# Kernel tuning notes

Measured on AMD Instinct MI355X. Metric: run time of the kernel, lower is better.

The kernel has to match this reference:

```python
import jax, jax.numpy as jnp
import numpy as np

N, E = 100000, 1600000
IN_CH, HID, HEADS, OUT_CH = 128, 32, 2, 40
NEG_SLOPE = 0.2
BN_EPS = 1e-5


def _param(key, shape, scale=0.1):
    return scale * jax.random.normal(key, shape, dtype=jnp.float32)


def setup_inputs() -> dict:
    key = jax.random.key(0)
    ks = jax.random.split(key, 24)
    x = jax.random.normal(ks[0], (N, IN_CH), dtype=jnp.float32)
    edge_index = jax.random.randint(ks[1], (2, E), 0, N, dtype=jnp.int32)
    d0 = HEADS * HID  # 64
    inp = {
        'x': x, 'edge_index': edge_index,
        # conv0: in 128 -> 32 per head, concat -> 64
        'W0': _param(ks[2], (IN_CH, HEADS * HID)),
        'as0': _param(ks[3], (HEADS, HID)), 'ad0': _param(ks[4], (HEADS, HID)),
        'b0': jnp.zeros((d0,), jnp.float32),
        'g0': jnp.ones((d0,), jnp.float32), 'bt0': jnp.zeros((d0,), jnp.float32),
        # conv1: 64 -> 32 per head, concat -> 64
        'W1': _param(ks[5], (d0, HEADS * HID)),
        'as1': _param(ks[6], (HEADS, HID)), 'ad1': _param(ks[7], (HEADS, HID)),
        'b1': jnp.zeros((d0,), jnp.float32),
        'g1': jnp.ones((d0,), jnp.float32), 'bt1': jnp.zeros((d0,), jnp.float32),
        # conv2: 64 -> 40 per head, mean over heads -> 40
        'W2': _param(ks[8], (d0, HEADS * OUT_CH)),
        'as2': _param(ks[9], (HEADS, OUT_CH)), 'ad2': _param(ks[10], (HEADS, OUT_CH)),
        'b2': jnp.zeros((OUT_CH,), jnp.float32),
    }
    return inp


def gat_conv(x, src, dst, W, a_src, a_dst, bias, out_ch, concat):
    n = x.shape[0]
    h = (x @ W).reshape(n, HEADS, out_ch)            # [N,H,C]
    alpha_src = jnp.sum(h * a_src, axis=-1)          # [N,H]
    alpha_dst = jnp.sum(h * a_dst, axis=-1)          # [N,H]
    e = jax.nn.leaky_relu(alpha_src[src] + alpha_dst[dst], NEG_SLOPE)  # [E,H]
    # softmax over incoming edges per destination node (self loops guarantee >=1 edge)
    m = jax.ops.segment_max(e, dst, num_segments=n)
    e = jnp.exp(e - m[dst])
    s = jax.ops.segment_sum(e, dst, num_segments=n)
    alpha = e / s[dst]                                # [E,H]
    msg = h[src] * alpha[:, :, None]                  # [E,H,C]
    out = jax.ops.segment_sum(msg, dst, num_segments=n)  # [N,H,C]
    out = out.reshape(n, HEADS * out_ch) if concat else out.mean(axis=1)
    return out + bias


def batch_norm(x, gamma, beta):
    mu = jnp.mean(x, axis=0)
    var = jnp.mean(jnp.square(x - mu), axis=0)
    return gamma * (x - mu) * jax.lax.rsqrt(var + BN_EPS) + beta


def reference(x, edge_index, W0, as0, ad0, b0, g0, bt0,
              W1, as1, ad1, b1, g1, bt1, W2, as2, ad2, b2):
    n = x.shape[0]
    loops = jnp.arange(n, dtype=edge_index.dtype)
    src = jnp.concatenate([edge_index[0], loops])
    dst = jnp.concatenate([edge_index[1], loops])
    h = gat_conv(x, src, dst, W0, as0, ad0, b0, HID, True)
    h = jax.nn.elu(batch_norm(h, g0, bt0))
    h = gat_conv(h, src, dst, W1, as1, ad1, b1, HID, True)
    h = jax.nn.elu(batch_norm(h, g1, bt1))
    return gat_conv(h, src, dst, W2, as2, ad2, b2, OUT_CH, False)
```

## Files before the change

kernel.cpp:

```cpp
#include <hip/hip_runtime.h>
#include <hip/hip_bf16.h>
#include <math.h>


#define NNODES 100000
#define NEDGES 1600000
#define ENTOT  (NEDGES + NNODES)
#define NEG_SLOPE 0.2f
#define BN_EPS 1e-5f

#define NRANGE 8
#define RSIZE  (NNODES/NRANGE)
#define BCAP   262144
#define PBLK   2048
#define NB2    32

typedef unsigned short u16;
typedef unsigned int u32;
typedef unsigned long long u64;
typedef __attribute__((ext_vector_type(8))) short short8;
typedef __attribute__((ext_vector_type(4))) float f32x4;

__device__ __forceinline__ float b2f(u16 u){ union{u32 i; float f;} v; v.i=((u32)u)<<16; return v.f; }
__device__ __forceinline__ u16 f2b(float x){ __hip_bfloat16 b=__float2bfloat16(x); return *(u16*)&b; }
__device__ __forceinline__ float ldf(const void* p, int i, int f){
  return f ? ((const float*)p)[i] : b2f(((const u16*)p)[i]);
}

__global__ void k_detect(const u16* __restrict__ x, int* __restrict__ flag){
  __shared__ int bad;
  if(threadIdx.x==0) bad=0;
  __syncthreads();
  int cnt=0;
  for(int i=threadIdx.x;i<4096;i+=256){
    u16 v = x[2*i];
    int ex = (v>>7)&0xff;
    if(ex==0xff || (ex==0 && (v&0x7fff)!=0)) cnt++;
  }
  atomicAdd(&bad,cnt);
  __syncthreads();
  if(threadIdx.x==0) flag[0] = (bad>4)?1:0;
}

__global__ __launch_bounds__(256) void k_part2(
    const int* __restrict__ ei, int* __restrict__ gptr, u32* __restrict__ bkt){
  __shared__ int lcnt[NRANGE], gbase[NRANGE];
  int t=threadIdx.x;
  if(t<NRANGE) lcnt[t]=0;
  __syncthreads();
  const int CH=(ENTOT+PBLK-1)/PBLK;
  int beg=blockIdx.x*CH, end=beg+CH; if(end>ENTOT) end=ENTOT;
  int nd[4], ns[4], nr[4], ne=0;
  for(int i=beg+t; i<end; i+=256){
    int d=(i<NEDGES)? ei[NEDGES+i] : (i-NEDGES);
    int s=(i<NEDGES)? ei[i] : d;
    nd[ne]=d; ns[ne]=s; ne++;
  }
  #pragma unroll 4
  for(int k=0;k<ne;k++) nr[k]=atomicAdd(&lcnt[nd[k]/RSIZE],1);
  __syncthreads();
  if(t<NRANGE) gbase[t]=atomicAdd(&gptr[t],lcnt[t]);
  __syncthreads();
  #pragma unroll 4
  for(int k=0;k<ne;k++){
    int r=nd[k]/RSIZE;
    u32 e = ((u32)(nd[k]-r*RSIZE)<<17) | (u32)ns[k];
    __builtin_nontemporal_store(e, &bkt[(size_t)r*BCAP + gbase[r] + nr[k]]);
  }
}

__global__ __launch_bounds__(256) void k_hist4(
    const u32* __restrict__ bkt, const int* __restrict__ gptr, int* __restrict__ lhist){
  __shared__ int lh[RSIZE];
  int t=threadIdx.x;
  for(int i=t;i<RSIZE;i+=256) lh[i]=0;
  __syncthreads();
  int r = blockIdx.x & (NRANGE-1);
  int c = blockIdx.x >> 3;
  int n = gptr[r];
  int per=(n+NB2-1)/NB2;
  int beg=c*per, end=beg+per; if(end>n) end=n;
  const u32* bp = bkt + (size_t)r*BCAP;
  for(int i=beg+t;i<end;i+=256) atomicAdd(&lh[bp[i]>>17],1);
  __syncthreads();
  int* out = lhist + (size_t)(r*NB2+c)*RSIZE;
  for(int i=t;i<RSIZE;i+=256) out[i]=lh[i];
}

__global__ __launch_bounds__(256) void k_sumscan(int* __restrict__ lhist, int* __restrict__ cnt){
  int n = blockIdx.x*256 + threadIdx.x;
  if(n>=NNODES) return;
  int r = n/RSIZE, i = n - r*RSIZE;
  int* base = lhist + (size_t)r*NB2*RSIZE + i;
  int run=0;
  #pragma unroll 8
  for(int c=0;c<NB2;c++){
    int v = base[(size_t)c*RSIZE];
    base[(size_t)c*RSIZE] = run;
    run += v;
  }
  cnt[n]=run;
}

#define SCAN_M (NNODES+1)
#define SCAN_NB ((SCAN_M + 2047)/2048)

__global__ void k_scan_a(const int* __restrict__ cnt, int* __restrict__ bsum){
  __shared__ int red[256];
  int b=blockIdx.x, t=threadIdx.x;
  int base = b*2048 + t*8;
  int s=0;
  #pragma unroll
  for(int j=0;j<8;j++){ int idx=base+j; s += (idx<NNODES)? cnt[idx]:0; }
  red[t]=s; __syncthreads();
  for(int o=128;o>0;o>>=1){ if(t<o) red[t]+=red[t+o]; __syncthreads(); }
  if(t==0) bsum[b]=red[0];
}

__global__ void k_scan_b(int* bsum){
  if(threadIdx.x==0){
    int run=0;
    for(int i=0;i<SCAN_NB;i++){ int v=bsum[i]; bsum[i]=run; run+=v; }
  }
}

__global__ void k_scan_c(const int* __restrict__ cnt, const int* __restrict__ bsum,
                         int* __restrict__ row_ptr){
  __shared__ int lds[256];
  int b=blockIdx.x, t=threadIdx.x;
  int base=b*2048+t*8;
  int v[8]; int s=0;
  #pragma unroll
  for(int j=0;j<8;j++){ int idx=base+j; int x=(idx<NNODES)?cnt[idx]:0; v[j]=s; s+=x; }
  lds[t]=s; __syncthreads();
  for(int o=1;o<256;o<<=1){
    int other=0; if(t>=o) other=lds[t-o];
    __syncthreads();
    lds[t]+=other;
    __syncthreads();
  }
  int texcl = lds[t] - s;
  int off0 = bsum[b] + texcl;
  #pragma unroll
  for(int j=0;j<8;j++){ int idx=base+j; if(idx<SCAN_M) row_ptr[idx]=off0+v[j]; }
}

__global__ __launch_bounds__(256) void k_scatter4(
    const u32* __restrict__ bkt, const int* __restrict__ gptr,
    const int* __restrict__ row_ptr, const int* __restrict__ lhist,
    int* __restrict__ col){
  __shared__ int lofs[RSIZE];
  int t=threadIdx.x;
  int r = blockIdx.x & (NRANGE-1);
  int c = blockIdx.x >> 3;
  int lo = r*RSIZE;
  const int* cb = lhist + (size_t)(r*NB2+c)*RSIZE;
  for(int i=t;i<RSIZE;i+=256) lofs[i] = row_ptr[lo+i] + cb[i];
  __syncthreads();
  int n = gptr[r];
  int per=(n+NB2-1)/NB2;
  int beg=c*per, end=beg+per; if(end>n) end=n;
  const u32* bp = bkt + (size_t)r*BCAP;
  for(int i=beg+t;i<end;i+=256){
    u32 e=bp[i];
    int pos=atomicAdd(&lofs[e>>17],1);
    col[pos]=(int)(e & 0x1FFFF);
  }
}

template<int K, int OUTC, int HID, bool XEXT, bool BN>
__global__ __launch_bounds__(256) void k_gemm_mfma(
    const void* __restrict__ xin, const void* __restrict__ W,
    const void* __restrict__ avs, const void* __restrict__ avd,
    const float2* __restrict__ bnab,
    u16* __restrict__ hout, float* __restrict__ asrc, float* __restrict__ adst,
    const int* __restrict__ flagp)
{
  const int f = flagp[0];
  constexpr int KP = K+8;
  constexpr int RS = OUTC+8;
  constexpr int NT = OUTC/16;
  constexpr int KQ = K/32;
  __shared__ __align__(16) u16 WT[OUTC*KP];
  __shared__ __align__(16) u16 HROW[4*16*RS];
  __shared__ float AVb[2*OUTC];
  __shared__ float2 BB[K];
  int t=threadIdx.x;
  const u16* Wu=(const u16*)W; const float* Wf=(const float*)W;
  for(int i8=t*8; i8<K*OUTC; i8+=256*8){
    int k=i8/OUTC, c0=i8-k*OUTC;
    u16 w8[8];
    if(f){
      const float* wp=Wf+i8;
      float4 a=*(const float4*)wp, b=*(const float4*)(wp+4);
      w8[0]=f2b(a.x);w8[1]=f2b(a.y);w8[2]=f2b(a.z);w8[3]=f2b(a.w);
      w8[4]=f2b(b.x);w8[5]=f2b(b.y);w8[6]=f2b(b.z);w8[7]=f2b(b.w);
    } else {
      uint4 q=*(const uint4*)(Wu+i8);
      w8[0]=q.x&0xffff;w8[1]=q.x>>16;w8[2]=q.y&0xffff;w8[3]=q.y>>16;
      w8[4]=q.z&0xffff;w8[5]=q.z>>16;w8[6]=q.w&0xffff;w8[7]=q.w>>16;
    }
    #pragma unroll
    for(int u=0;u<8;u++) WT[(c0+u)*KP + k] = w8[u];
  }
  for(int idx=t; idx<2*OUTC; idx+=256)
    AVb[idx] = (idx<OUTC)? ldf(avs,idx,f) : ldf(avd,idx-OUTC,f);
  if(BN) for(int idx=t; idx<K; idx+=256) BB[idx]=bnab[idx];
  __syncthreads();

  int wv=t>>6, lane=t&63;
  int m=lane&15, quad=lane>>4;
  int grow0 = blockIdx.x*64 + wv*16;
  int growA = grow0 + m;
  bool avalid = growA < NNODES;
  int growC = avalid ? growA : 0;

  f32x4 acc[NT] = {};
  #pragma unroll
  for(int kq=0;kq<KQ;kq++){
    int k0 = kq*32 + quad*8;
    union{ u32 u[4]; short8 s8; } A;
    if(XEXT && f==1){
      const float* xr=(const float*)xin + (size_t)growC*K + k0;
      float4 p=*(const float4*)xr, q=*(const float4*)(xr+4);
      A.u[0]=f2b(p.x)|((u32)f2b(p.y)<<16);
      A.u[1]=f2b(p.z)|((u32)f2b(p.w)<<16);
      A.u[2]=f2b(q.x)|((u32)f2b(q.y)<<16);
      A.u[3]=f2b(q.z)|((u32)f2b(q.w)<<16);
    } else {
      uint4 q=*(const uint4*)((const u16*)xin + (size_t)growC*K + k0);
      A.u[0]=q.x; A.u[1]=q.y; A.u[2]=q.z; A.u[3]=q.w;
    }
    if(BN){
      #pragma unroll
      for(int j=0;j<4;j++){
        float lo=b2f(A.u[j]&0xffff), hi=b2f(A.u[j]>>16);
        float2 c1=BB[k0+2*j], c2=BB[k0+2*j+1];
        lo=c1.x*lo+c1.y; lo = lo>0.f? lo : __expf(lo)-1.f;
        hi=c2.x*hi+c2.y; hi = hi>0.f? hi : __expf(hi)-1.f;
        A.u[j]=f2b(lo)|((u32)f2b(hi)<<16);
      }
    }
    #pragma unroll
    for(int nt=0;nt<NT;nt++){
      union{ uint4 q; short8 s8; } Bf;
      Bf.q = *(const uint4*)&WT[(nt*16+m)*KP + k0];
      acc[nt] = __builtin_amdgcn_mfma_f32_16x16x32_bf16(A.s8, Bf.s8, acc[nt], 0,0,0);
    }
  }
  u16* hr = &HROW[wv*16*RS];
  #pragma unroll
  for(int nt=0;nt<NT;nt++){
    #pragma unroll
    for(int reg=0;reg<4;reg++)
      hr[(quad*4+reg)*RS + nt*16+m] = f2b(acc[nt][reg]);
  }
  __syncthreads();
  {
    int row=lane&15, task=quad, head=task&1, sd=task>>1;
    float p=0.f;
    const u16* hrow=&hr[row*RS + head*HID];
    const float* av=&AVb[sd*OUTC + head*HID];
    #pragma unroll 8
    for(int c=0;c<HID;c++) p += b2f(hrow[c])*av[c];
    int grow=grow0+row;
    if(grow<NNODES){ (sd? adst:asrc)[grow*2+head]=p; }
  }
  {
    constexpr int CH8 = OUTC/8;
    for(int idx=lane; idx<16*CH8; idx+=64){
      int rr=idx/CH8, c8=idx-rr*CH8;
      int grow=grow0+rr;
      if(grow<NNODES)
        *(uint4*)(hout + (size_t)grow*OUTC + c8*8) = *(const uint4*)&hr[rr*RS + c8*8];
    }
  }
}

template<int OUTC, bool FINAL>
__global__ __launch_bounds__(256) void k_aggf(
  const int* __restrict__ row_ptr, const int* __restrict__ col,
  const u16* __restrict__ hin, const float2* __restrict__ asrc2,
  const float2* __restrict__ adst2, const void* __restrict__ bias,
  u16* __restrict__ houtb, void* __restrict__ outv, const int* __restrict__ flagp)
{
  const int f = flagp[0];
  __shared__ float vbuf[4][80];
  int wave = threadIdx.x>>6, lane=threadIdx.x&63;
  int rr = blockIdx.x & 7, jb = blockIdx.x >> 3;
  int d = rr*RSIZE + jb*4 + wave;
  int base=row_ptr[d], deg=row_ptr[d+1]-base;
  int slot=lane>>3, cg=lane&7;
  constexpr int HSPLIT = FINAL ? 5 : 4;
  float2 adv = adst2[d];
  float acc[8]={0,0,0,0,0,0,0,0}, accx[2]={0.f,0.f};
  float s0=0.f, s1=0.f;
  for(int j=0;j<deg;j+=8){
    int jj=j+slot;
    bool valid = jj<deg;
    int cs = col[base + (valid? jj : 0)];
    if(valid){
      float2 sv = asrc2[cs];
      float e0=sv.x+adv.x; e0 = e0>0.f? e0 : NEG_SLOPE*e0; e0=fminf(e0,60.f);
      float e1=sv.y+adv.y; e1 = e1>0.f? e1 : NEG_SLOPE*e1; e1=fminf(e1,60.f);
      float p0=__expf(e0), p1=__expf(e1);
      s0+=p0; s1+=p1;
      const u16* hp = hin + (size_t)cs*OUTC;
      uint4 hq = *(const uint4*)(hp + cg*8);
      float p = (cg<HSPLIT)? p0 : p1;
      acc[0]+=p*b2f(hq.x&0xffff); acc[1]+=p*b2f(hq.x>>16);
      acc[2]+=p*b2f(hq.y&0xffff); acc[3]+=p*b2f(hq.y>>16);
      acc[4]+=p*b2f(hq.z&0xffff); acc[5]+=p*b2f(hq.z>>16);
      acc[6]+=p*b2f(hq.w&0xffff); acc[7]+=p*b2f(hq.w>>16);
      if(FINAL){
        ushort2 hc = *(const ushort2*)(hp + 64 + cg*2);
        accx[0]+=p1*b2f(hc.x); accx[1]+=p1*b2f(hc.y);
      }
    }
  }
  #pragma unroll
  for(int o=8;o<64;o<<=1){
    s0+=__shfl_xor(s0,o,64); s1+=__shfl_xor(s1,o,64);
    #pragma unroll
    for(int k=0;k<8;k++) acc[k]+=__shfl_xor(acc[k],o,64);
    if(FINAL){ accx[0]+=__shfl_xor(accx[0],o,64); accx[1]+=__shfl_xor(accx[1],o,64); }
  }
  float inv0 = s0>0.f?1.f/s0:0.f, inv1 = s1>0.f?1.f/s1:0.f;
  if(!FINAL){
    if(slot==0){
      float inv = (cg<4)? inv0 : inv1;
      u16 o8[8];
      #pragma unroll
      for(int k=0;k<8;k++) o8[k]=f2b(acc[k]*inv + ldf(bias,cg*8+k,f));
      uint4 ov;
      ov.x=(u32)o8[0]|((u32)o8[1]<<16); ov.y=(u32)o8[2]|((u32)o8[3]<<16);
      ov.z=(u32)o8[4]|((u32)o8[5]<<16); ov.w=(u32)o8[6]|((u32)o8[7]<<16);
      *(uint4*)(houtb + (size_t)d*64 + cg*8) = ov;
    }
  } else {
    if(slot==0){
      #pragma unroll
      for(int k=0;k<8;k++){
        int ch=cg*8+k;
        vbuf[wave][ch] = acc[k]*((ch<40)?inv0:inv1);
      }
      vbuf[wave][64+cg*2]   = accx[0]*inv1;
      vbuf[wave][64+cg*2+1] = accx[1]*inv1;
    }
    __syncthreads();
    if(lane<40){
      float res = 0.5f*(vbuf[wave][lane] + vbuf[wave][40+lane]) + ldf(bias,lane,f);
      if(f) ((float*)outv)[(size_t)d*40+lane] = res;
      else  ((__hip_bfloat16*)outv)[(size_t)d*40+lane] = __float2bfloat16(res);
    }
  }
}

__global__ __launch_bounds__(256) void k_bnstats(const u16* __restrict__ h, float* __restrict__ stats){
  __shared__ float red[4][128];
  int t=threadIdx.x; int c=t&63; int g=t>>6;
  float s=0.f,q=0.f;
  for(int r=blockIdx.x*4+g; r<NNODES; r+=gridDim.x*4){
    float v=b2f(h[(size_t)r*64+c]); s+=v; q+=v*v;
  }
  red[g][c]=s; red[g][64+c]=q;
  __syncthreads();
  if(t<128){
    float tot=red[0][t]+red[1][t]+red[2][t]+red[3][t];
    atomicAdd(&stats[t], tot);
  }
}

__global__ void k_bnfinal(const float* __restrict__ stats,
                          const void* __restrict__ gm, const void* __restrict__ bt,
                          float2* __restrict__ bnab, const int* __restrict__ flagp){
  const int f = flagp[0];
  int c=threadIdx.x;
  if(c>=64) return;
  float mu=stats[c]*(1.0f/NNODES);
  float var=stats[64+c]*(1.0f/NNODES)-mu*mu;
  var = var>0.f?var:0.f;
  float A = ldf(gm,c,f)*rsqrtf(var+BN_EPS);
  float B = ldf(bt,c,f) - A*mu;
  bnab[c]=make_float2(A,B);
}

extern "C" void kernel_launch(void* const* d_in, const int* in_sizes, int n_in,
                              void* d_out, int out_size, void* d_ws, size_t ws_size,
                              hipStream_t stream){
  const void* x  =d_in[0];
  const int* ei =(const int*)d_in[1];
  const void* W0 =d_in[2];  const void* as0=d_in[3];  const void* ad0=d_in[4];
  const void* b0 =d_in[5];  const void* g0 =d_in[6];  const void* bt0=d_in[7];
  const void* W1 =d_in[8];  const void* as1=d_in[9];  const void* ad1=d_in[10];
  const void* b1 =d_in[11]; const void* g1 =d_in[12]; const void* bt1=d_in[13];
  const void* W2 =d_in[14]; const void* as2=d_in[15]; const void* ad2=d_in[16];
  const void* b2 =d_in[17];

  char* ws=(char*)d_ws;
  size_t off=0;
  auto alloc=[&](size_t bytes)->void*{ void* p=ws+off; off+=(bytes+255)&~(size_t)255; return p; };
  int*    flag   =(int*)   alloc(256);
  int*    row_ptr=(int*)   alloc((size_t)(NNODES+1)*4);
  int*    cnt    =(int*)   alloc((size_t)NNODES*4);
  int*    colx   =(int*)   alloc((size_t)ENTOT*4);
  int*    bsum   =(int*)   alloc((size_t)SCAN_NB*4);
  int*    gptr   =(int*)   alloc(256);
  u32*    bkt    =(u32*)   alloc((size_t)NRANGE*BCAP*4);
  u16*    hA     =(u16*)   alloc((size_t)100032*80*2);
  u16*    hB0    =(u16*)   alloc((size_t)100032*64*2);
  u16*    hB1    =(u16*)   alloc((size_t)100032*64*2);
  float*  asrc   =(float*) alloc((size_t)NNODES*2*4);
  float*  adst   =(float*) alloc((size_t)NNODES*2*4);
  float*  stats  =(float*) alloc(128*4);
  float2* bnab   =(float2*)alloc(64*8);
  int*    lhist  =(int*)hA;

  k_detect<<<1,256,0,stream>>>((const u16*)x, flag);

  (void)hipMemsetAsync(gptr,0,256,stream);
  k_part2  <<<PBLK,256,0,stream>>>(ei,gptr,bkt);
  k_hist4  <<<NRANGE*NB2,256,0,stream>>>(bkt,gptr,lhist);
  k_sumscan<<<(NNODES+255)/256,256,0,stream>>>(lhist,cnt);
  k_scan_a <<<SCAN_NB,256,0,stream>>>(cnt,bsum);
  k_scan_b <<<1,64,0,stream>>>(bsum);
  k_scan_c <<<SCAN_NB,256,0,stream>>>(cnt,bsum,row_ptr);
  k_scatter4<<<NRANGE*NB2,256,0,stream>>>(bkt,gptr,row_ptr,lhist,colx);

  int gG = (NNODES+63)/64;
  int gN = NNODES/4;
  k_gemm_mfma<128,64,32,true ,false><<<gG,256,0,stream>>>(
      x,W0,as0,ad0,nullptr,hA,asrc,adst,flag);
  k_aggf<64,false><<<gN,256,0,stream>>>(row_ptr,colx,hA,
      (const float2*)asrc,(const float2*)adst,b0,hB0,nullptr,flag);
  (void)hipMemsetAsync(stats,0,512,stream);
  k_bnstats<<<256,256,0,stream>>>(hB0,stats);
  k_bnfinal<<<1,64,0,stream>>>(stats,g0,bt0,bnab,flag);
  k_gemm_mfma<64,64,32,false,true ><<<gG,256,0,stream>>>(
      hB0,W1,as1,ad1,bnab,hA,asrc,adst,flag);
  k_aggf<64,false><<<gN,256,0,stream>>>(row_ptr,colx,hA,
      (const float2*)asrc,(const float2*)adst,b1,hB1,nullptr,flag);
  (void)hipMemsetAsync(stats,0,512,stream);
  k_bnstats<<<256,256,0,stream>>>(hB1,stats);
  k_bnfinal<<<1,64,0,stream>>>(stats,g1,bt1,bnab,flag);
  k_gemm_mfma<64,80,40,false,true ><<<gG,256,0,stream>>>(
      hB1,W2,as2,ad2,bnab,hA,asrc,adst,flag);
  k_aggf<80,true ><<<gN,256,0,stream>>>(row_ptr,colx,hA,
      (const float2*)asrc,(const float2*)adst,b2,nullptr,d_out,flag);

  (void)in_sizes;(void)n_in;(void)out_size;(void)ws_size;
}
```

Before: 483.6 us.

## Bucket edges by destination and source range to sort columns within rows

The partition pass now buckets edges into 64 buckets keyed by both destination range and source range, instead of 8 destination-only buckets. The histogram, prefix-sum and scatter kernels walk the source-range buckets in order, so each CSR row's column list ends up grouped by source range. This is meant to improve gather locality in the aggregation kernels, which read h[src] rows. The cost is more buckets, smaller fixed capacity per bucket (40960, which could overflow on skewed inputs), and an extra loop level in the prefix sum.

```diff
diff --git a/kernel.cpp b/kernel.cpp
--- a/kernel.cpp
+++ b/kernel.cpp
@@ -11,9 +11,10 @@
 
 #define NRANGE 8
 #define RSIZE  (NNODES/NRANGE)
-#define BCAP   262144
+#define NBKT   64
+#define BCAP   40960
 #define PBLK   2048
-#define NB2    32
+#define NCH    4
 
 typedef unsigned short u16;
 typedef unsigned int u32;
@@ -44,29 +45,29 @@
 
 __global__ __launch_bounds__(256) void k_part2(
     const int* __restrict__ ei, int* __restrict__ gptr, u32* __restrict__ bkt){
-  __shared__ int lcnt[NRANGE], gbase[NRANGE];
+  __shared__ int lcnt[NBKT], gbase[NBKT];
   int t=threadIdx.x;
-  if(t<NRANGE) lcnt[t]=0;
+  if(t<NBKT) lcnt[t]=0;
   __syncthreads();
   const int CH=(ENTOT+PBLK-1)/PBLK;
   int beg=blockIdx.x*CH, end=beg+CH; if(end>ENTOT) end=ENTOT;
-  int nd[4], ns[4], nr[4], ne=0;
+  int nb[4], nr[4]; u32 nv[4]; int ne=0;
   for(int i=beg+t; i<end; i+=256){
     int d=(i<NEDGES)? ei[NEDGES+i] : (i-NEDGES);
     int s=(i<NEDGES)? ei[i] : d;
-    nd[ne]=d; ns[ne]=s; ne++;
+    int rd=d/RSIZE, rs=s/RSIZE;
+    nb[ne]=rd*NRANGE+rs;
+    nv[ne]=((u32)(d-rd*RSIZE)<<17)|(u32)s;
+    ne++;
   }
   #pragma unroll 4
-  for(int k=0;k<ne;k++) nr[k]=atomicAdd(&lcnt[nd[k]/RSIZE],1);
-  __syncthreads();
-  if(t<NRANGE) gbase[t]=atomicAdd(&gptr[t],lcnt[t]);
+  for(int k=0;k<ne;k++) nr[k]=atomicAdd(&lcnt[nb[k]],1);
+  __syncthreads();
+  if(t<NBKT) gbase[t]=atomicAdd(&gptr[t],lcnt[t]);
   __syncthreads();
   #pragma unroll 4
-  for(int k=0;k<ne;k++){
-    int r=nd[k]/RSIZE;
-    u32 e = ((u32)(nd[k]-r*RSIZE)<<17) | (u32)ns[k];
-    __builtin_nontemporal_store(e, &bkt[(size_t)r*BCAP + gbase[r] + nr[k]]);
-  }
+  for(int k=0;k<ne;k++)
+    __builtin_nontemporal_store(nv[k], &bkt[(size_t)nb[k]*BCAP + gbase[nb[k]] + nr[k]]);
 }
 
 __global__ __launch_bounds__(256) void k_hist4(
@@ -75,29 +76,32 @@
   int t=threadIdx.x;
   for(int i=t;i<RSIZE;i+=256) lh[i]=0;
   __syncthreads();
-  int r = blockIdx.x & (NRANGE-1);
-  int c = blockIdx.x >> 3;
-  int n = gptr[r];
-  int per=(n+NB2-1)/NB2;
+  int rd=blockIdx.x&7, rs=(blockIdx.x>>3)&7, c=blockIdx.x>>6;
+  int b = rd*NRANGE+rs;
+  int n = gptr[b];
+  int per=(n+NCH-1)/NCH;
   int beg=c*per, end=beg+per; if(end>n) end=n;
-  const u32* bp = bkt + (size_t)r*BCAP;
+  const u32* bp = bkt + (size_t)b*BCAP;
   for(int i=beg+t;i<end;i+=256) atomicAdd(&lh[bp[i]>>17],1);
   __syncthreads();
-  int* out = lhist + (size_t)(r*NB2+c)*RSIZE;
+  int* out = lhist + (size_t)(b*NCH+c)*RSIZE;
   for(int i=t;i<RSIZE;i+=256) out[i]=lh[i];
 }
 
 __global__ __launch_bounds__(256) void k_sumscan(int* __restrict__ lhist, int* __restrict__ cnt){
   int n = blockIdx.x*256 + threadIdx.x;
   if(n>=NNODES) return;
-  int r = n/RSIZE, i = n - r*RSIZE;
-  int* base = lhist + (size_t)r*NB2*RSIZE + i;
+  int rd = n/RSIZE, i = n - rd*RSIZE;
   int run=0;
-  #pragma unroll 8
-  for(int c=0;c<NB2;c++){
-    int v = base[(size_t)c*RSIZE];
-    base[(size_t)c*RSIZE] = run;
-    run += v;
+  #pragma unroll 4
+  for(int rs=0;rs<NRANGE;rs++){
+    int* base = lhist + (size_t)((rd*NRANGE+rs)*NCH)*RSIZE + i;
+    #pragma unroll
+    for(int c=0;c<NCH;c++){
+      int v = base[(size_t)c*RSIZE];
+      base[(size_t)c*RSIZE] = run;
+      run += v;
+    }
   }
   cnt[n]=run;
 }
@@ -151,16 +155,16 @@
     int* __restrict__ col){
   __shared__ int lofs[RSIZE];
   int t=threadIdx.x;
-  int r = blockIdx.x & (NRANGE-1);
-  int c = blockIdx.x >> 3;
-  int lo = r*RSIZE;
-  const int* cb = lhist + (size_t)(r*NB2+c)*RSIZE;
+  int rd=blockIdx.x&7, rs=(blockIdx.x>>3)&7, c=blockIdx.x>>6;
+  int b = rd*NRANGE+rs;
+  int lo = rd*RSIZE;
+  const int* cb = lhist + (size_t)(b*NCH+c)*RSIZE;
   for(int i=t;i<RSIZE;i+=256) lofs[i] = row_ptr[lo+i] + cb[i];
   __syncthreads();
-  int n = gptr[r];
-  int per=(n+NB2-1)/NB2;
+  int n = gptr[b];
+  int per=(n+NCH-1)/NCH;
   int beg=c*per, end=beg+per; if(end>n) end=n;
-  const u32* bp = bkt + (size_t)r*BCAP;
+  const u32* bp = bkt + (size_t)b*BCAP;
   for(int i=beg+t;i<end;i+=256){
     u32 e=bp[i];
     int pos=atomicAdd(&lofs[e>>17],1);
@@ -406,7 +410,7 @@
   int*    colx   =(int*)   alloc((size_t)ENTOT*4);
   int*    bsum   =(int*)   alloc((size_t)SCAN_NB*4);
   int*    gptr   =(int*)   alloc(256);
-  u32*    bkt    =(u32*)   alloc((size_t)NRANGE*BCAP*4);
+  u32*    bkt    =(u32*)   alloc((size_t)NBKT*BCAP*4);
   u16*    hA     =(u16*)   alloc((size_t)100032*80*2);
   u16*    hB0    =(u16*)   alloc((size_t)100032*64*2);
   u16*    hB1    =(u16*)   alloc((size_t)100032*64*2);
@@ -420,12 +424,12 @@
 
   (void)hipMemsetAsync(gptr,0,256,stream);
   k_part2  <<<PBLK,256,0,stream>>>(ei,gptr,bkt);
-  k_hist4  <<<NRANGE*NB2,256,0,stream>>>(bkt,gptr,lhist);
+  k_hist4  <<<NBKT*NCH,256,0,stream>>>(bkt,gptr,lhist);
   k_sumscan<<<(NNODES+255)/256,256,0,stream>>>(lhist,cnt);
   k_scan_a <<<SCAN_NB,256,0,stream>>>(cnt,bsum);
   k_scan_b <<<1,64,0,stream>>>(bsum);
   k_scan_c <<<SCAN_NB,256,0,stream>>>(cnt,bsum,row_ptr);
-  k_scatter4<<<NRANGE*NB2,256,0,stream>>>(bkt,gptr,row_ptr,lhist,colx);
+  k_scatter4<<<NBKT*NCH,256,0,stream>>>(bkt,gptr,row_ptr,lhist,colx);
 
   int gG = (NNODES+63)/64;
   int gN = NNODES/4;
```

Measured after the change: 526.0 us. 8.8% more time.
